# Kernel tuning notes

Measured on AMD Instinct MI355X. Metric: run time of the kernel, lower is better.

Reference implementation:

```python
import jax, jax.numpy as jnp
import numpy as np

HIDDEN = 512
QK_DIM = HIDDEN // 8  # 64
B, H, W = 32, 32, 32


def conv1x1(x, w, b):
    # 1x1 conv == channel matmul: w [out_c, in_c], x [b, in_c, h, w]
    return jnp.einsum('oc,bchw->bohw', w, x) + b[None, :, None, None]


def setup_inputs() -> dict:
    key = jax.random.key(0)
    ks = jax.random.split(key, 10)
    s = 0.02
    return {
        'x': jax.random.normal(ks[0], (B, HIDDEN, H, W), jnp.float32),
        'pos_embedding': jax.random.normal(ks[1], (1, HIDDEN, 32, 32), jnp.float32),
        'query_w': jax.random.normal(ks[2], (QK_DIM, HIDDEN), jnp.float32) * s,
        'query_b': jax.random.normal(ks[3], (QK_DIM,), jnp.float32) * s,
        'key_w': jax.random.normal(ks[4], (QK_DIM, HIDDEN), jnp.float32) * s,
        'key_b': jax.random.normal(ks[5], (QK_DIM,), jnp.float32) * s,
        'value_w': jax.random.normal(ks[6], (HIDDEN, HIDDEN), jnp.float32) * s,
        'value_b': jax.random.normal(ks[7], (HIDDEN,), jnp.float32) * s,
        'out_w': jax.random.normal(ks[8], (HIDDEN, HIDDEN), jnp.float32) * s,
        'out_b': jax.random.normal(ks[9], (HIDDEN,), jnp.float32) * s,
    }


def reference(x, pos_embedding, query_w, query_b, key_w, key_b,
              value_w, value_b, out_w, out_b):
    b, c, h, w = x.shape
    n = h * w
    x = x + pos_embedding[:, :, :h, :w]
    q = conv1x1(x, query_w, query_b).reshape(b, -1, n)   # [b, d, n]
    k = conv1x1(x, key_w, key_b).reshape(b, -1, n)       # [b, d, n]
    v = conv1x1(x, value_w, value_b).reshape(b, -1, n)   # [b, c, n]
    # scores[b,i,j] = sum_d q[b,d,i] * k[b,d,j]  (no 1/sqrt(d) scaling, faithful)
    scores = jnp.einsum('bdi,bdj->bij', q, k)
    attn = jax.nn.softmax(scores, axis=-1)               # [b, n, n]
    # out[b,c,i] = sum_j v[b,c,j] * attn[b,i,j]
    out = jnp.einsum('bcj,bij->bci', v, attn).reshape(b, c, h, w)
    return conv1x1(out, out_w, out_b)
```

## Files before the change

kernel.cpp:

```cpp
#include <hip/hip_runtime.h>

#define BB 32
#define CC 512
#define DD 64
#define NN 1024
#define GRP 16
#define NGRP (BB / GRP)

typedef float4 f4;
typedef __attribute__((ext_vector_type(8))) short bf16x8;
typedef __attribute__((ext_vector_type(4))) float f32x4;
typedef __attribute__((ext_vector_type(4))) unsigned short us4;
typedef __attribute__((ext_vector_type(8))) unsigned short us8;

__device__ inline unsigned short bf16rn(float f) {
  union { float f; unsigned u; } v; v.f = f;
  unsigned r = v.u + 0x7fff + ((v.u >> 16) & 1);
  return (unsigned short)(r >> 16);
}

__device__ inline void gl_lds16(const void* g, void* l) {
  __builtin_amdgcn_global_load_lds(
      (const __attribute__((address_space(1))) unsigned int*)g,
      (__attribute__((address_space(3))) unsigned int*)l, 16, 0, 0);
}

__device__ inline void wait_prefetch_and_barrier() {
  asm volatile("s_waitcnt vmcnt(0)" ::: "memory");
  __builtin_amdgcn_s_barrier();
}

template <int KDIM>
__device__ inline void gemm_core(const unsigned short* __restrict__ A,
                                 const unsigned short* __restrict__ Bt,
                                 int m0, int n0, int tid,
                                 unsigned short* sA, unsigned short* sB,
                                 f32x4 acc[4][4]) {
  const int wave = tid >> 6, lane = tid & 63;
  const int wm = (wave & 1) * 64, wn = (wave >> 1) * 64;
  const int fm = lane & 15;
  const int kq = lane >> 4;
  const int srow = lane >> 3;
  const int sg   = (lane & 7) ^ srow;

  const unsigned short* ga = A  + (size_t)(m0 + srow) * KDIM + sg * 8;
  const unsigned short* gb = Bt + (size_t)(n0 + srow) * KDIM + sg * 8;

  auto stage = [&](int buf, int k0) {
#pragma unroll
    for (int t = 0; t < 4; ++t) {
      const int R = wave * 32 + t * 8;
      gl_lds16(ga + (size_t)R * KDIM + k0, sA + buf * 8192 + R * 64);
      gl_lds16(gb + (size_t)R * KDIM + k0, sB + buf * 8192 + R * 64);
    }
  };

  stage(0, 0);
  wait_prefetch_and_barrier();

  int cur = 0;
  for (int k0 = 0; k0 < KDIM; k0 += 64) {
    if (k0 + 64 < KDIM) stage(cur ^ 1, k0 + 64);
    const unsigned short* pA = sA + cur * 8192;
    const unsigned short* pB = sB + cur * 8192;
#pragma unroll
    for (int ks = 0; ks < 2; ++ks) {
      bf16x8 af[4], bfr[4];
#pragma unroll
      for (int i = 0; i < 4; ++i) {
        const int ra = wm + i * 16 + fm;
        const int rb = wn + i * 16 + fm;
        af[i]  = *(const bf16x8*)(pA + ra * 64 + ((ks * 4 + kq) ^ (ra & 7)) * 8);
        bfr[i] = *(const bf16x8*)(pB + rb * 64 + ((ks * 4 + kq) ^ (rb & 7)) * 8);
      }
#pragma unroll
      for (int i = 0; i < 4; ++i)
#pragma unroll
        for (int j = 0; j < 4; ++j)
          acc[i][j] = __builtin_amdgcn_mfma_f32_16x16x32_bf16(af[i], bfr[j], acc[i][j], 0, 0, 0);
    }
    wait_prefetch_and_barrier();
    cur ^= 1;
  }
}

__global__ __launch_bounds__(256) void prep_w(
    const float* __restrict__ qw, const float* __restrict__ kw, const float* __restrict__ vw,
    const float* __restrict__ qb, const float* __restrict__ kb, const float* __restrict__ vb,
    const float* __restrict__ ow,
    unsigned short* __restrict__ wcat, unsigned short* __restrict__ owb,
    float* __restrict__ bcat) {
  int idx = blockIdx.x * 256 + threadIdx.x;
  if (idx < 640 * 512) {
    int row = idx >> 9;
    float v = (row < 64) ? qw[idx] : (row < 128) ? kw[idx - 64 * 512] : vw[idx - 128 * 512];
    wcat[idx] = bf16rn(v);
    if (idx < 640) bcat[idx] = (idx < 64) ? qb[idx] : (idx < 128) ? kb[idx - 64] : vb[idx - 128];
  } else {
    int j = idx - 640 * 512;
    owb[j] = bf16rn(ow[j]);
  }
}

__global__ __launch_bounds__(256) void prep_x(const float* __restrict__ x,
                                              const float* __restrict__ pos,
                                              unsigned short* __restrict__ A) {
  __shared__ float t[64][65];
  const int b = blockIdx.z, i0 = blockIdx.x * 64, c0 = blockIdx.y * 64;
  const int tid = threadIdx.x;
  const int ci = tid >> 4, il = (tid & 15) * 4;
  const float* xb = x + (size_t)b * CC * NN;
#pragma unroll
  for (int r = 0; r < 4; ++r) {
    int cl = r * 16 + ci;
    f4 xv = *(const f4*)(xb  + (size_t)(c0 + cl) * NN + i0 + il);
    f4 pv = *(const f4*)(pos + (size_t)(c0 + cl) * NN + i0 + il);
    t[cl][il + 0] = xv.x + pv.x;
    t[cl][il + 1] = xv.y + pv.y;
    t[cl][il + 2] = xv.z + pv.z;
    t[cl][il + 3] = xv.w + pv.w;
  }
  __syncthreads();
  const int iw = tid >> 2, cw = (tid & 3) * 16;
  unsigned short* dst = A + ((size_t)b * NN + i0 + iw) * CC + c0 + cw;
  us8 p0, p1;
#pragma unroll
  for (int j = 0; j < 8; ++j) p0[j] = bf16rn(t[cw + j][iw]);
#pragma unroll
  for (int j = 0; j < 8; ++j) p1[j] = bf16rn(t[cw + 8 + j][iw]);
  *(us8*)dst = p0;
  *(us8*)(dst + 8) = p1;
}

__global__ __launch_bounds__(256) void proj_gemm(
    const unsigned short* __restrict__ A, const unsigned short* __restrict__ wcat,
    const float* __restrict__ bcat,
    unsigned short* __restrict__ qo, unsigned short* __restrict__ ko,
    unsigned short* __restrict__ vto) {
  __shared__ unsigned short sA[16384], sB[16384];
  const int b = blockIdx.z, m0 = blockIdx.x * 128, n0 = blockIdx.y * 128;
  const int tid = threadIdx.x, wave = tid >> 6, lane = tid & 63;
  f32x4 acc[4][4];
#pragma unroll
  for (int i = 0; i < 4; ++i)
#pragma unroll
    for (int j = 0; j < 4; ++j) acc[i][j] = (f32x4)(0.0f);

  gemm_core<512>(A + (size_t)b * NN * CC, wcat, m0, n0, tid, sA, sB, acc);

  const int wm = (wave & 1) * 64, wn = (wave >> 1) * 64;
#pragma unroll
  for (int i = 0; i < 4; ++i)
#pragma unroll
    for (int j = 0; j < 4; ++j) {
      int col  = n0 + wn + j * 16 + (lane & 15);
      int rowb = m0 + wm + i * 16 + (lane >> 4) * 4;
      float bias = bcat[col];
      if (col < 64) {
#pragma unroll
        for (int r = 0; r < 4; ++r)
          qo[((size_t)b * NN + rowb + r) * DD + col] = bf16rn(acc[i][j][r] + bias);
      } else if (col < 128) {
#pragma unroll
        for (int r = 0; r < 4; ++r)
          ko[((size_t)b * NN + rowb + r) * DD + col - 64] = bf16rn(acc[i][j][r] + bias);
      } else {
        int c = col - 128;
        us4 pk;
#pragma unroll
        for (int r = 0; r < 4; ++r) pk[r] = bf16rn(acc[i][j][r] + bias);
        *(us4*)(vto + ((size_t)b * CC + c) * NN + rowb) = pk;
      }
    }
}

__global__ __launch_bounds__(256) void stats_kernel(
    const unsigned short* __restrict__ q, const unsigned short* __restrict__ k,
    float2* __restrict__ stats) {
  __shared__ unsigned short sQ[8192];
  __shared__ unsigned short sK[16384];
  __shared__ float2 wred[4][128];

  const int b = blockIdx.y, i0 = blockIdx.x * 128;
  const int tid = threadIdx.x, wave = tid >> 6, lane = tid & 63;
  const int wm = (wave & 1) * 64, wn = (wave >> 1) * 64;
  const int fm = lane & 15, kq = lane >> 4;
  const int srow = lane >> 3, sg = (lane & 7) ^ srow;

  const unsigned short* qb = q + (size_t)b * NN * DD;
  const unsigned short* kb = k + (size_t)b * NN * DD;

  auto stageK = [&](int buf, int j0) {
#pragma unroll
    for (int t = 0; t < 4; ++t) {
      const int R = wave * 32 + t * 8;
      gl_lds16(kb + (size_t)(j0 + R + srow) * DD + sg * 8, sK + buf * 8192 + R * 64);
    }
  };

#pragma unroll
  for (int t = 0; t < 4; ++t) {
    const int R = wave * 32 + t * 8;
    gl_lds16(qb + (size_t)(i0 + R + srow) * DD + sg * 8, sQ + R * 64);
  }
  stageK(0, 0);
  wait_prefetch_and_barrier();

  bf16x8 aq[4][2];
#pragma unroll
  for (int i = 0; i < 4; ++i)
#pragma unroll
    for (int kd = 0; kd < 2; ++kd) {
      const int ra = wm + i * 16 + fm;
      aq[i][kd] = *(const bf16x8*)(sQ + ra * 64 + ((kd * 4 + kq) ^ (ra & 7)) * 8);
    }

  float m_l[4][4], l_l[4][4];
#pragma unroll
  for (int i = 0; i < 4; ++i)
#pragma unroll
    for (int r = 0; r < 4; ++r) { m_l[i][r] = -1e30f; l_l[i][r] = 0.f; }

  int cur = 0;
  for (int jt = 0; jt < 8; ++jt) {
    if (jt < 7) stageK(cur ^ 1, (jt + 1) * 128);
    const unsigned short* pK = sK + cur * 8192;
    f32x4 S[4][4];
#pragma unroll
    for (int i = 0; i < 4; ++i)
#pragma unroll
      for (int j = 0; j < 4; ++j) S[i][j] = (f32x4)(0.0f);
#pragma unroll
    for (int kd = 0; kd < 2; ++kd) {
      bf16x8 bk[4];
#pragma unroll
      for (int j = 0; j < 4; ++j) {
        const int rb = wn + j * 16 + fm;
        bk[j] = *(const bf16x8*)(pK + rb * 64 + ((kd * 4 + kq) ^ (rb & 7)) * 8);
      }
#pragma unroll
      for (int i = 0; i < 4; ++i)
#pragma unroll
        for (int j = 0; j < 4; ++j)
          S[i][j] = __builtin_amdgcn_mfma_f32_16x16x32_bf16(aq[i][kd], bk[j], S[i][j], 0, 0, 0);
    }
#pragma unroll
    for (int i = 0; i < 4; ++i)
#pragma unroll
      for (int r = 0; r < 4; ++r) {
        float v0 = S[i][0][r], v1 = S[i][1][r], v2 = S[i][2][r], v3 = S[i][3][r];
        float mt = fmaxf(fmaxf(v0, v1), fmaxf(v2, v3));
        float lt = __expf(v0 - mt) + __expf(v1 - mt) + __expf(v2 - mt) + __expf(v3 - mt);
        float mo = m_l[i][r];
        float mn = fmaxf(mo, mt);
        l_l[i][r] = l_l[i][r] * __expf(mo - mn) + lt * __expf(mt - mn);
        m_l[i][r] = mn;
      }
    wait_prefetch_and_barrier();
    cur ^= 1;
  }

#pragma unroll
  for (int i = 0; i < 4; ++i)
#pragma unroll
    for (int r = 0; r < 4; ++r) {
      float m = m_l[i][r], l = l_l[i][r];
#pragma unroll
      for (int off = 1; off < 16; off <<= 1) {
        float mo = __shfl_xor(m, off, 64);
        float lo = __shfl_xor(l, off, 64);
        float mn = fmaxf(m, mo);
        l = l * __expf(m - mn) + lo * __expf(mo - mn);
        m = mn;
      }
      m_l[i][r] = m; l_l[i][r] = l;
    }
  if ((lane & 15) == 0) {
#pragma unroll
    for (int i = 0; i < 4; ++i)
#pragma unroll
      for (int r = 0; r < 4; ++r) {
        float2 p; p.x = m_l[i][r]; p.y = l_l[i][r];
        wred[wave][wm + i * 16 + kq * 4 + r] = p;
      }
  }
  __syncthreads();
  if (tid < 128) {
    const int a = tid >> 6;
    float2 p0 = wred[a][tid], p1 = wred[a + 2][tid];
    float mn = fmaxf(p0.x, p1.x);
    float l = p0.y * __expf(p0.x - mn) + p1.y * __expf(p1.x - mn);
    float2 o; o.x = mn; o.y = l;
    stats[(size_t)b * NN + i0 + tid] = o;
  }
}

__global__ __launch_bounds__(256) void pnorm_kernel(
    const unsigned short* __restrict__ q, const unsigned short* __restrict__ k,
    const float2* __restrict__ stats, unsigned short* __restrict__ P) {
  __shared__ unsigned short sQ[8192];
  __shared__ unsigned short sK[16384];

  const int b = blockIdx.y, i0 = blockIdx.x * 128;
  const int tid = threadIdx.x, wave = tid >> 6, lane = tid & 63;
  const int wm = (wave & 1) * 64, wn = (wave >> 1) * 64;
  const int fm = lane & 15, kq = lane >> 4;
  const int srow = lane >> 3, sg = (lane & 7) ^ srow;

  const unsigned short* qb = q + (size_t)b * NN * DD;
  const unsigned short* kb = k + (size_t)b * NN * DD;

  auto stageK = [&](int buf, int j0) {
#pragma unroll
    for (int t = 0; t < 4; ++t) {
      const int R = wave * 32 + t * 8;
      gl_lds16(kb + (size_t)(j0 + R + srow) * DD + sg * 8, sK + buf * 8192 + R * 64);
    }
  };

#pragma unroll
  for (int t = 0; t < 4; ++t) {
    const int R = wave * 32 + t * 8;
    gl_lds16(qb + (size_t)(i0 + R + srow) * DD + sg * 8, sQ + R * 64);
  }
  stageK(0, 0);

  float mrow[4][4], irow[4][4];
#pragma unroll
  for (int i = 0; i < 4; ++i)
#pragma unroll
    for (int r = 0; r < 4; ++r) {
      float2 st = stats[(size_t)b * NN + i0 + wm + i * 16 + kq * 4 + r];
      mrow[i][r] = st.x; irow[i][r] = 1.0f / st.y;
    }

  wait_prefetch_and_barrier();

  bf16x8 aq[4][2];
#pragma unroll
  for (int i = 0; i < 4; ++i)
#pragma unroll
    for (int kd = 0; kd < 2; ++kd) {
      const int ra = wm + i * 16 + fm;
      aq[i][kd] = *(const bf16x8*)(sQ + ra * 64 + ((kd * 4 + kq) ^ (ra & 7)) * 8);
    }

  int cur = 0;
  for (int jt = 0; jt < 8; ++jt) {
    const int j0 = jt * 128;
    if (jt < 7) stageK(cur ^ 1, j0 + 128);
    const unsigned short* pK = sK + cur * 8192;
    f32x4 S[4][4];
#pragma unroll
    for (int i = 0; i < 4; ++i)
#pragma unroll
      for (int j = 0; j < 4; ++j) S[i][j] = (f32x4)(0.0f);
#pragma unroll
    for (int kd = 0; kd < 2; ++kd) {
      bf16x8 bk[4];
#pragma unroll
      for (int j = 0; j < 4; ++j) {
        const int rb = wn + j * 16 + fm;
        bk[j] = *(const bf16x8*)(pK + rb * 64 + ((kd * 4 + kq) ^ (rb & 7)) * 8);
      }
#pragma unroll
      for (int i = 0; i < 4; ++i)
#pragma unroll
        for (int j = 0; j < 4; ++j)
          S[i][j] = __builtin_amdgcn_mfma_f32_16x16x32_bf16(aq[i][kd], bk[j], S[i][j], 0, 0, 0);
    }
#pragma unroll
    for (int i = 0; i < 4; ++i)
#pragma unroll
      for (int j = 0; j < 4; ++j)
#pragma unroll
        for (int r = 0; r < 4; ++r)
          S[i][j][r] = __expf(S[i][j][r] - mrow[i][r]) * irow[i][r];

    wait_prefetch_and_barrier();

#pragma unroll
    for (int i = 0; i < 4; ++i)
#pragma unroll
      for (int j = 0; j < 4; ++j) {
        const int col = j0 + wn + j * 16 + fm;
#pragma unroll
        for (int r = 0; r < 4; ++r) {
          const int row = i0 + wm + i * 16 + kq * 4 + r;
          P[((size_t)b * NN + row) * NN + col] = bf16rn(S[i][j][r]);
        }
      }
    cur ^= 1;
  }
}

__global__ __launch_bounds__(256) void pv_gemm(
    const unsigned short* __restrict__ P, const unsigned short* __restrict__ vT,
    unsigned short* __restrict__ attnout) {
  __shared__ unsigned short sA[16384], sB[16384];
  const int b = blockIdx.z, m0 = blockIdx.x * 128, n0 = blockIdx.y * 128;
  const int tid = threadIdx.x, wave = tid >> 6, lane = tid & 63;
  f32x4 acc[4][4];
#pragma unroll
  for (int i = 0; i < 4; ++i)
#pragma unroll
    for (int j = 0; j < 4; ++j) acc[i][j] = (f32x4)(0.0f);

  gemm_core<1024>(P + (size_t)b * NN * NN, vT + (size_t)b * CC * NN, m0, n0, tid, sA, sB, acc);

  const int wm = (wave & 1) * 64, wn = (wave >> 1) * 64;
#pragma unroll
  for (int i = 0; i < 4; ++i)
#pragma unroll
    for (int j = 0; j < 4; ++j) {
      int col  = n0 + wn + j * 16 + (lane & 15);
      int rowb = m0 + wm + i * 16 + (lane >> 4) * 4;
#pragma unroll
      for (int r = 0; r < 4; ++r)
        attnout[((size_t)b * NN + rowb + r) * CC + col] = bf16rn(acc[i][j][r]);
    }
}

__global__ __launch_bounds__(256) void outproj_gemm(
    const unsigned short* __restrict__ owb, const unsigned short* __restrict__ attnout,
    const float* __restrict__ ob, float* __restrict__ out) {
  __shared__ unsigned short sA[16384], sB[16384];
  const int b = blockIdx.z, m0 = blockIdx.x * 128, n0 = blockIdx.y * 128;
  const int tid = threadIdx.x, wave = tid >> 6, lane = tid & 63;
  f32x4 acc[4][4];
#pragma unroll
  for (int i = 0; i < 4; ++i)
#pragma unroll
    for (int j = 0; j < 4; ++j) acc[i][j] = (f32x4)(0.0f);

  gemm_core<512>(owb, attnout + (size_t)b * NN * CC, m0, n0, tid, sA, sB, acc);

  const int wm = (wave & 1) * 64, wn = (wave >> 1) * 64;
#pragma unroll
  for (int i = 0; i < 4; ++i)
#pragma unroll
    for (int j = 0; j < 4; ++j) {
      int col  = n0 + wn + j * 16 + (lane & 15);
      int rowb = m0 + wm + i * 16 + (lane >> 4) * 4;
      f4 b4 = *(const f4*)(ob + rowb);
#pragma unroll
      for (int r = 0; r < 4; ++r)
        out[((size_t)b * CC + rowb + r) * NN + col] = acc[i][j][r] + ((const float*)&b4)[r];
    }
}

extern "C" void kernel_launch(void* const* d_in, const int* in_sizes, int n_in,
                              void* d_out, int out_size, void* d_ws, size_t ws_size,
                              hipStream_t stream) {
  const float* x   = (const float*)d_in[0];
  const float* pos = (const float*)d_in[1];
  const float* qw  = (const float*)d_in[2];
  const float* qb  = (const float*)d_in[3];
  const float* kw  = (const float*)d_in[4];
  const float* kb  = (const float*)d_in[5];
  const float* vw  = (const float*)d_in[6];
  const float* vb  = (const float*)d_in[7];
  const float* ow  = (const float*)d_in[8];
  const float* ob  = (const float*)d_in[9];
  float* out = (float*)d_out;

  char* w = (char*)d_ws;
  unsigned short* wcat = (unsigned short*)w; w += (size_t)640 * 512 * 2;
  unsigned short* owb  = (unsigned short*)w; w += (size_t)512 * 512 * 2;
  float*          bcat = (float*)w;          w += 640 * 4;
  unsigned short* A    = (unsigned short*)w; w += (size_t)BB * NN * CC * 2;
  unsigned short* q    = (unsigned short*)w; w += (size_t)BB * NN * DD * 2;
  unsigned short* k    = (unsigned short*)w; w += (size_t)BB * NN * DD * 2;
  unsigned short* vT   = (unsigned short*)w; w += (size_t)BB * CC * NN * 2;
  float2*        stats = (float2*)w;         w += (size_t)BB * NN * 8;
  unsigned short* PG   = (unsigned short*)w; w += (size_t)GRP * NN * NN * 2;
  unsigned short* attnout = A;

  hipLaunchKernelGGL(prep_w, dim3(2304), dim3(256), 0, stream,
                     qw, kw, vw, qb, kb, vb, ow, wcat, owb, bcat);
  hipLaunchKernelGGL(prep_x, dim3(16, 8, 32), dim3(256), 0, stream, x, pos, A);
  hipLaunchKernelGGL(proj_gemm, dim3(8, 5, 32), dim3(256), 0, stream,
                     A, wcat, bcat, q, k, vT);
  hipLaunchKernelGGL(stats_kernel, dim3(8, 32), dim3(256), 0, stream, q, k, stats);

  for (int g = 0; g < NGRP; ++g) {
    const unsigned short* qg  = q  + (size_t)g * GRP * NN * DD;
    const unsigned short* kg  = k  + (size_t)g * GRP * NN * DD;
    const unsigned short* vTg = vT + (size_t)g * GRP * CC * NN;
    const float2*         stg = stats + (size_t)g * GRP * NN;
    unsigned short* aog = attnout + (size_t)g * GRP * NN * CC;
    hipLaunchKernelGGL(pnorm_kernel, dim3(8, GRP), dim3(256), 0, stream, qg, kg, stg, PG);
    hipLaunchKernelGGL(pv_gemm, dim3(8, 4, GRP), dim3(256), 0, stream, PG, vTg, aog);
  }

  hipLaunchKernelGGL(outproj_gemm, dim3(4, 8, 32), dim3(256), 0, stream,
                     owb, attnout, ob, out);
}
```

Before: 321.5 us.

## Fuse softmax normalization with PV GEMM, split stats over keys, add XCD swizzle

Replaces the pnorm_kernel and pv_gemm pair, which wrote a full bf16 probability matrix to global memory in two batch groups, with a fused flash_pv kernel. It recomputes QK^T per tile, normalizes using precomputed stats, stages P in LDS and multiplies by V tiles in place. The stats kernel is split into two key halves to double its grid, and the partials are merged in flash_pv. All GEMM grids are flattened with an XCD-aware block swizzle for L2 locality. In exchange, QK^T is recomputed once per channel block (four times), and the larger LDS footprint limits the kernel to one block per CU.

```diff
diff --git a/kernel.cpp b/kernel.cpp
--- a/kernel.cpp
+++ b/kernel.cpp
@@ -4,8 +4,6 @@
 #define CC 512
 #define DD 64
 #define NN 1024
-#define GRP 16
-#define NGRP (BB / GRP)
 
 typedef float4 f4;
 typedef __attribute__((ext_vector_type(8))) short bf16x8;
@@ -25,9 +23,13 @@
       (__attribute__((address_space(3))) unsigned int*)l, 16, 0, 0);
 }
 
-__device__ inline void wait_prefetch_and_barrier() {
+__device__ inline void wait_vm0_barrier() {
   asm volatile("s_waitcnt vmcnt(0)" ::: "memory");
   __builtin_amdgcn_s_barrier();
+}
+
+__device__ inline int xcd_swz(int bid, int nwg) {
+  return (bid & 7) * (nwg >> 3) + (bid >> 3);
 }
 
 template <int KDIM>
@@ -56,7 +58,7 @@
   };
 
   stage(0, 0);
-  wait_prefetch_and_barrier();
+  wait_vm0_barrier();
 
   int cur = 0;
   for (int k0 = 0; k0 < KDIM; k0 += 64) {
@@ -79,7 +81,7 @@
         for (int j = 0; j < 4; ++j)
           acc[i][j] = __builtin_amdgcn_mfma_f32_16x16x32_bf16(af[i], bfr[j], acc[i][j], 0, 0, 0);
     }
-    wait_prefetch_and_barrier();
+    wait_vm0_barrier();
     cur ^= 1;
   }
 }
@@ -138,7 +140,8 @@
     unsigned short* __restrict__ qo, unsigned short* __restrict__ ko,
     unsigned short* __restrict__ vto) {
   __shared__ unsigned short sA[16384], sB[16384];
-  const int b = blockIdx.z, m0 = blockIdx.x * 128, n0 = blockIdx.y * 128;
+  const int wid = xcd_swz(blockIdx.x, 1280);
+  const int m0 = (wid & 7) * 128, n0 = ((wid >> 3) % 5) * 128, b = wid / 40;
   const int tid = threadIdx.x, wave = tid >> 6, lane = tid & 63;
   f32x4 acc[4][4];
 #pragma unroll
@@ -176,12 +179,14 @@
 
 __global__ __launch_bounds__(256) void stats_kernel(
     const unsigned short* __restrict__ q, const unsigned short* __restrict__ k,
-    float2* __restrict__ stats) {
+    float2* __restrict__ stats_part) {
   __shared__ unsigned short sQ[8192];
   __shared__ unsigned short sK[16384];
   __shared__ float2 wred[4][128];
 
-  const int b = blockIdx.y, i0 = blockIdx.x * 128;
+  const int wid = xcd_swz(blockIdx.x, 512);
+  const int i0 = (wid & 7) * 128, jc = (wid >> 3) & 1, b = wid >> 4;
+  const int jbase = jc * 512;
   const int tid = threadIdx.x, wave = tid >> 6, lane = tid & 63;
   const int wm = (wave & 1) * 64, wn = (wave >> 1) * 64;
   const int fm = lane & 15, kq = lane >> 4;
@@ -203,8 +208,8 @@
     const int R = wave * 32 + t * 8;
     gl_lds16(qb + (size_t)(i0 + R + srow) * DD + sg * 8, sQ + R * 64);
   }
-  stageK(0, 0);
-  wait_prefetch_and_barrier();
+  stageK(0, jbase);
+  wait_vm0_barrier();
 
   bf16x8 aq[4][2];
 #pragma unroll
@@ -222,8 +227,9 @@
     for (int r = 0; r < 4; ++r) { m_l[i][r] = -1e30f; l_l[i][r] = 0.f; }
 
   int cur = 0;
-  for (int jt = 0; jt < 8; ++jt) {
-    if (jt < 7) stageK(cur ^ 1, (jt + 1) * 128);
+#pragma unroll
+  for (int jt = 0; jt < 4; ++jt) {
+    if (jt < 3) stageK(cur ^ 1, jbase + (jt + 1) * 128);
     const unsigned short* pK = sK + cur * 8192;
     f32x4 S[4][4];
 #pragma unroll
@@ -256,7 +262,7 @@
         l_l[i][r] = l_l[i][r] * __expf(mo - mn) + lt * __expf(mt - mn);
         m_l[i][r] = mn;
       }
-    wait_prefetch_and_barrier();
+    wait_vm0_barrier();
     cur ^= 1;
   }
 
@@ -291,24 +297,30 @@
     float mn = fmaxf(p0.x, p1.x);
     float l = p0.y * __expf(p0.x - mn) + p1.y * __expf(p1.x - mn);
     float2 o; o.x = mn; o.y = l;
-    stats[(size_t)b * NN + i0 + tid] = o;
-  }
-}
-
-__global__ __launch_bounds__(256) void pnorm_kernel(
+    stats_part[((size_t)b * NN + i0 + tid) * 2 + jc] = o;
+  }
+}
+
+__global__ __launch_bounds__(256, 1) void flash_pv(
     const unsigned short* __restrict__ q, const unsigned short* __restrict__ k,
-    const float2* __restrict__ stats, unsigned short* __restrict__ P) {
+    const unsigned short* __restrict__ vT, const float2* __restrict__ stats_part,
+    unsigned short* __restrict__ attnout) {
   __shared__ unsigned short sQ[8192];
   __shared__ unsigned short sK[16384];
-
-  const int b = blockIdx.y, i0 = blockIdx.x * 128;
+  __shared__ unsigned short sV[32768];
+  __shared__ unsigned short sP[16384];
+
+  const int wid = xcd_swz(blockIdx.x, 1024);
+  const int c0 = (wid & 3) * 128, i0 = ((wid >> 2) & 7) * 128, b = wid >> 5;
   const int tid = threadIdx.x, wave = tid >> 6, lane = tid & 63;
   const int wm = (wave & 1) * 64, wn = (wave >> 1) * 64;
   const int fm = lane & 15, kq = lane >> 4;
   const int srow = lane >> 3, sg = (lane & 7) ^ srow;
-
-  const unsigned short* qb = q + (size_t)b * NN * DD;
-  const unsigned short* kb = k + (size_t)b * NN * DD;
+  const int vrow = lane >> 4, vg = lane & 15;
+
+  const unsigned short* qb = q  + (size_t)b * NN * DD;
+  const unsigned short* kb = k  + (size_t)b * NN * DD;
+  const unsigned short* vb = vT + (size_t)b * CC * NN;
 
   auto stageK = [&](int buf, int j0) {
 #pragma unroll
@@ -317,6 +329,15 @@
       gl_lds16(kb + (size_t)(j0 + R + srow) * DD + sg * 8, sK + buf * 8192 + R * 64);
     }
   };
+  auto stageV = [&](int buf, int j0) {
+#pragma unroll
+    for (int t = 0; t < 8; ++t) {
+      const int R4 = (wave * 8 + t) * 4;
+      const int row = R4 + vrow;
+      gl_lds16(vb + (size_t)(c0 + row) * NN + j0 + ((vg ^ (row & 7)) << 3),
+               sV + buf * 16384 + (wave * 8 + t) * 512);
+    }
+  };
 
 #pragma unroll
   for (int t = 0; t < 4; ++t) {
@@ -324,32 +345,41 @@
     gl_lds16(qb + (size_t)(i0 + R + srow) * DD + sg * 8, sQ + R * 64);
   }
   stageK(0, 0);
+  stageV(0, 0);
 
   float mrow[4][4], irow[4][4];
 #pragma unroll
   for (int i = 0; i < 4; ++i)
 #pragma unroll
     for (int r = 0; r < 4; ++r) {
-      float2 st = stats[(size_t)b * NN + i0 + wm + i * 16 + kq * 4 + r];
-      mrow[i][r] = st.x; irow[i][r] = 1.0f / st.y;
-    }
-
-  wait_prefetch_and_barrier();
+      const size_t row = (size_t)b * NN + i0 + wm + i * 16 + kq * 4 + r;
+      f4 st = *(const f4*)(stats_part + row * 2);
+      float m = fmaxf(st.x, st.z);
+      float l = st.y * __expf(st.x - m) + st.w * __expf(st.z - m);
+      mrow[i][r] = m; irow[i][r] = 1.0f / l;
+    }
 
   bf16x8 aq[4][2];
-#pragma unroll
-  for (int i = 0; i < 4; ++i)
-#pragma unroll
-    for (int kd = 0; kd < 2; ++kd) {
-      const int ra = wm + i * 16 + fm;
-      aq[i][kd] = *(const bf16x8*)(sQ + ra * 64 + ((kd * 4 + kq) ^ (ra & 7)) * 8);
-    }
-
-  int cur = 0;
+  f32x4 acc[4][4];
+#pragma unroll
+  for (int i = 0; i < 4; ++i)
+#pragma unroll
+    for (int j = 0; j < 4; ++j) acc[i][j] = (f32x4)(0.0f);
+
+  int buf = 0;
   for (int jt = 0; jt < 8; ++jt) {
-    const int j0 = jt * 128;
-    if (jt < 7) stageK(cur ^ 1, j0 + 128);
-    const unsigned short* pK = sK + cur * 8192;
+    wait_vm0_barrier();
+    if (jt < 7) { stageK(buf ^ 1, (jt + 1) * 128); stageV(buf ^ 1, (jt + 1) * 128); }
+    if (jt == 0) {
+#pragma unroll
+      for (int i = 0; i < 4; ++i)
+#pragma unroll
+        for (int kd = 0; kd < 2; ++kd) {
+          const int ra = wm + i * 16 + fm;
+          aq[i][kd] = *(const bf16x8*)(sQ + ra * 64 + ((kd * 4 + kq) ^ (ra & 7)) * 8);
+        }
+    }
+    const unsigned short* pK = sK + buf * 8192;
     f32x4 S[4][4];
 #pragma unroll
     for (int i = 0; i < 4; ++i)
@@ -372,52 +402,50 @@
 #pragma unroll
     for (int i = 0; i < 4; ++i)
 #pragma unroll
-      for (int j = 0; j < 4; ++j)
-#pragma unroll
-        for (int r = 0; r < 4; ++r)
-          S[i][j][r] = __expf(S[i][j][r] - mrow[i][r]) * irow[i][r];
-
-    wait_prefetch_and_barrier();
-
-#pragma unroll
-    for (int i = 0; i < 4; ++i)
-#pragma unroll
-      for (int j = 0; j < 4; ++j) {
-        const int col = j0 + wn + j * 16 + fm;
+      for (int jj = 0; jj < 4; ++jj) {
+        const int col = wn + jj * 16 + fm;
+        const int g = col >> 3, o = col & 7;
 #pragma unroll
         for (int r = 0; r < 4; ++r) {
-          const int row = i0 + wm + i * 16 + kq * 4 + r;
-          P[((size_t)b * NN + row) * NN + col] = bf16rn(S[i][j][r]);
+          const int row = wm + i * 16 + kq * 4 + r;
+          sP[row * 128 + ((g ^ (row & 7)) << 3) + o] =
+              bf16rn(__expf(S[i][jj][r] - mrow[i][r]) * irow[i][r]);
         }
       }
-    cur ^= 1;
-  }
-}
-
-__global__ __launch_bounds__(256) void pv_gemm(
-    const unsigned short* __restrict__ P, const unsigned short* __restrict__ vT,
-    unsigned short* __restrict__ attnout) {
-  __shared__ unsigned short sA[16384], sB[16384];
-  const int b = blockIdx.z, m0 = blockIdx.x * 128, n0 = blockIdx.y * 128;
-  const int tid = threadIdx.x, wave = tid >> 6, lane = tid & 63;
-  f32x4 acc[4][4];
-#pragma unroll
-  for (int i = 0; i < 4; ++i)
-#pragma unroll
-    for (int j = 0; j < 4; ++j) acc[i][j] = (f32x4)(0.0f);
-
-  gemm_core<1024>(P + (size_t)b * NN * NN, vT + (size_t)b * CC * NN, m0, n0, tid, sA, sB, acc);
-
-  const int wm = (wave & 1) * 64, wn = (wave >> 1) * 64;
-#pragma unroll
-  for (int i = 0; i < 4; ++i)
-#pragma unroll
-    for (int j = 0; j < 4; ++j) {
-      int col  = n0 + wn + j * 16 + (lane & 15);
-      int rowb = m0 + wm + i * 16 + (lane >> 4) * 4;
+    asm volatile("s_waitcnt lgkmcnt(0)" ::: "memory");
+    __builtin_amdgcn_s_barrier();
+    const unsigned short* pV = sV + buf * 16384;
+#pragma unroll
+    for (int kd = 0; kd < 4; ++kd) {
+      bf16x8 pa[4], vv[4];
+#pragma unroll
+      for (int i = 0; i < 4; ++i) {
+        const int ra = wm + i * 16 + fm;
+        pa[i] = *(const bf16x8*)(sP + ra * 128 + (((kd * 4 + kq) ^ (ra & 7)) << 3));
+      }
+#pragma unroll
+      for (int jj = 0; jj < 4; ++jj) {
+        const int rb = wn + jj * 16 + fm;
+        vv[jj] = *(const bf16x8*)(pV + rb * 128 + (((kd * 4 + kq) ^ (rb & 7)) << 3));
+      }
+#pragma unroll
+      for (int i = 0; i < 4; ++i)
+#pragma unroll
+        for (int jj = 0; jj < 4; ++jj)
+          acc[i][jj] = __builtin_amdgcn_mfma_f32_16x16x32_bf16(pa[i], vv[jj], acc[i][jj], 0, 0, 0);
+    }
+    buf ^= 1;
+  }
+
+#pragma unroll
+  for (int i = 0; i < 4; ++i)
+#pragma unroll
+    for (int jj = 0; jj < 4; ++jj) {
+      int col  = c0 + wn + jj * 16 + fm;
+      int rowb = i0 + wm + i * 16 + kq * 4;
 #pragma unroll
       for (int r = 0; r < 4; ++r)
-        attnout[((size_t)b * NN + rowb + r) * CC + col] = bf16rn(acc[i][j][r]);
+        attnout[((size_t)b * NN + rowb + r) * CC + col] = bf16rn(acc[i][jj][r]);
     }
 }
 
@@ -425,7 +453,8 @@
     const unsigned short* __restrict__ owb, const unsigned short* __restrict__ attnout,
     const float* __restrict__ ob, float* __restrict__ out) {
   __shared__ unsigned short sA[16384], sB[16384];
-  const int b = blockIdx.z, m0 = blockIdx.x * 128, n0 = blockIdx.y * 128;
+  const int wid = xcd_swz(blockIdx.x, 1024);
+  const int m0 = (wid & 3) * 128, n0 = ((wid >> 2) & 7) * 128, b = wid >> 5;
   const int tid = threadIdx.x, wave = tid >> 6, lane = tid & 63;
   f32x4 acc[4][4];
 #pragma unroll
@@ -472,27 +501,17 @@
   unsigned short* q    = (unsigned short*)w; w += (size_t)BB * NN * DD * 2;
   unsigned short* k    = (unsigned short*)w; w += (size_t)BB * NN * DD * 2;
   unsigned short* vT   = (unsigned short*)w; w += (size_t)BB * CC * NN * 2;
-  float2*        stats = (float2*)w;         w += (size_t)BB * NN * 8;
-  unsigned short* PG   = (unsigned short*)w; w += (size_t)GRP * NN * NN * 2;
+  float2*    stats_prt = (float2*)w;         w += (size_t)BB * NN * 2 * 8;
   unsigned short* attnout = A;
 
   hipLaunchKernelGGL(prep_w, dim3(2304), dim3(256), 0, stream,
                      qw, kw, vw, qb, kb, vb, ow, wcat, owb, bcat);
   hipLaunchKernelGGL(prep_x, dim3(16, 8, 32), dim3(256), 0, stream, x, pos, A);
-  hipLaunchKernelGGL(proj_gemm, dim3(8, 5, 32), dim3(256), 0, stream,
+  hipLaunchKernelGGL(proj_gemm, dim3(1280), dim3(256), 0, stream,
                      A, wcat, bcat, q, k, vT);
-  hipLaunchKernelGGL(stats_kernel, dim3(8, 32), dim3(256), 0, stream, q, k, stats);
-
-  for (int g = 0; g < NGRP; ++g) {
-    const unsigned short* qg  = q  + (size_t)g * GRP * NN * DD;
-    const unsigned short* kg  = k  + (size_t)g * GRP * NN * DD;
-    const unsigned short* vTg = vT + (size_t)g * GRP * CC * NN;
-    const float2*         stg = stats + (size_t)g * GRP * NN;
-    unsigned short* aog = attnout + (size_t)g * GRP * NN * CC;
-    hipLaunchKernelGGL(pnorm_kernel, dim3(8, GRP), dim3(256), 0, stream, qg, kg, stg, PG);
-    hipLaunchKernelGGL(pv_gemm, dim3(8, 4, GRP), dim3(256), 0, stream, PG, vTg, aog);
-  }
-
-  hipLaunchKernelGGL(outproj_gemm, dim3(4, 8, 32), dim3(256), 0, stream,
+  hipLaunchKernelGGL(stats_kernel, dim3(512), dim3(256), 0, stream, q, k, stats_prt);
+  hipLaunchKernelGGL(flash_pv, dim3(1024), dim3(256), 0, stream,
+                     q, k, vT, stats_prt, attnout);
+  hipLaunchKernelGGL(outproj_gemm, dim3(1024), dim3(256), 0, stream,
                      owb, attnout, ob, out);
 }
```

Measured after the change: 340.1 us. 1.06x slower.
